# Performance work log

Hardware: AMD Instinct MI355X
Metric: run time of the kernel (lower is better)

Reference implementation:

```python
import jax, jax.numpy as jnp
import numpy as np

CHI, CHO, K, PAD = 64, 64, 3, 1
EPS = 1e-5


def setup_inputs() -> dict:
    key = jax.random.key(0)
    ks = jax.random.split(key, 4)
    B, H, W = 4, 128, 128
    x = jax.random.normal(ks[0], (B, CHI, H, W), jnp.float32)
    # conv_offset: produces 3*dg*K*K = 27 channels (o1, o2, mask); init small so offsets are modest
    w_off = jax.random.normal(ks[1], (3 * K * K, CHI, K, K), jnp.float32) * 0.01
    b_off = jnp.zeros((3 * K * K,), jnp.float32)
    # main deformable conv weight/bias
    w = jax.random.normal(ks[2], (CHO, CHI, K, K), jnp.float32) * (1.0 / np.sqrt(CHI * K * K))
    b = jnp.zeros((CHO,), jnp.float32)
    # BatchNorm affine params
    gamma = jnp.ones((CHO,), jnp.float32)
    beta = jnp.zeros((CHO,), jnp.float32)
    return {"x": x, "w_off": w_off, "b_off": b_off, "w": w, "b": b, "gamma": gamma, "beta": beta}


def _deform_conv(x, w_off, b_off, w, b):
    B, C, H, W_ = x.shape
    # offset/mask prediction: plain 3x3 conv, pad 1 -> [B, 27, H, W]
    off = jax.lax.conv_general_dilated(
        x, w_off, (1, 1), ((PAD, PAD), (PAD, PAD)),
        dimension_numbers=("NCHW", "OIHW", "NCHW")) + b_off[None, :, None, None]
    o1, o2, m = jnp.split(off, 3, axis=1)
    # mmcv DCNv2: offset = cat(o1, o2) -> [B, 2*K*K, H, W], interleaved (dy, dx) per tap
    offset = jnp.concatenate([o1, o2], axis=1).reshape(B, K * K, 2, H, W_)
    mask = jax.nn.sigmoid(m)                      # [B, 9, H, W]
    dy, dx = offset[:, :, 0], offset[:, :, 1]     # [B, 9, H, W]

    ky, kx = jnp.meshgrid(jnp.arange(K), jnp.arange(K), indexing="ij")
    ky = ky.reshape(1, K * K, 1, 1).astype(x.dtype)
    kx = kx.reshape(1, K * K, 1, 1).astype(x.dtype)
    hh = jnp.arange(H, dtype=x.dtype).reshape(1, 1, H, 1)
    ww = jnp.arange(W_, dtype=x.dtype).reshape(1, 1, 1, W_)
    py = hh - PAD + ky + dy                       # sampling row coords [B,9,H,W]
    px = ww - PAD + kx + dx                       # sampling col coords [B,9,H,W]

    y0 = jnp.floor(py)
    x0 = jnp.floor(px)
    wy = py - y0
    wx = px - x0

    x_flat = x.reshape(B, C, H * W_)

    def gather(yi, xi):
        # bilinear corner gather with zero padding outside the feature map
        valid = ((yi >= 0) & (yi < H) & (xi >= 0) & (xi < W_)).astype(x.dtype)
        yc = jnp.clip(yi, 0, H - 1).astype(jnp.int32)
        xc = jnp.clip(xi, 0, W_ - 1).astype(jnp.int32)
        idx = (yc * W_ + xc).reshape(B, 1, -1)
        v = jnp.take_along_axis(x_flat, idx, axis=2).reshape(B, C, K * K, H, W_)
        return v * valid[:, None]

    v00 = gather(y0, x0)
    v01 = gather(y0, x0 + 1)
    v10 = gather(y0 + 1, x0)
    v11 = gather(y0 + 1, x0 + 1)

    wy_ = wy[:, None]
    wx_ = wx[:, None]
    val = (v00 * (1 - wy_) * (1 - wx_) + v01 * (1 - wy_) * wx_
           + v10 * wy_ * (1 - wx_) + v11 * wy_ * wx_)
    val = val * mask[:, None]                     # modulated sampling [B,C,9,H,W]

    out = jnp.einsum("bckhw,ock->bohw", val, w.reshape(CHO, CHI, K * K))
    return out + b[None, :, None, None]


def reference(x, w_off, b_off, w, b, gamma, beta):
    y = _deform_conv(x, w_off, b_off, w, b)
    # BatchNorm2d (training-mode forward: batch statistics, biased variance)
    mean = y.mean(axis=(0, 2, 3))
    var = y.var(axis=(0, 2, 3))
    yhat = (y - mean[None, :, None, None]) * jax.lax.rsqrt(var[None, :, None, None] + EPS)
    return jax.nn.relu(yhat * gamma[None, :, None, None] + beta[None, :, None, None])
```

## Files before the change

### kernel.cpp

```cpp
#include <hip/hip_runtime.h>
#include <math.h>

#define CHI 64
#define CHO 64
#define HH 128
#define WW 128
#define NB 4
#define KK 9
#define NOFF 27
#define EPSV 1e-5f
#define PLANE (HH * WW)
#define SP 72

typedef float f32x4 __attribute__((ext_vector_type(4)));
typedef short bf16x8 __attribute__((ext_vector_type(8)));
typedef unsigned int u32x4 __attribute__((ext_vector_type(4)));

__device__ __forceinline__ unsigned short f2bf(float f) {
    unsigned u = __float_as_uint(f);
    u += 0x7fff + ((u >> 16) & 1);
    return (unsigned short)(u >> 16);
}
__device__ __forceinline__ float bfl(unsigned u) { return __uint_as_float(u << 16); }
__device__ __forceinline__ float bfh(unsigned u) { return __uint_as_float(u & 0xffff0000u); }

__global__ __launch_bounds__(256) void transpose_kernel(const float* __restrict__ x,
                                                        unsigned short* __restrict__ x_bf) {
    const int id = blockIdx.x;
    const int b  = id >> 7;
    const int y  = id & 127;
    const int t  = threadIdx.x;
    __shared__ unsigned short lt[128 * SP];

    const int ci = t >> 2, qx = t & 3;
    const float* src = x + ((size_t)(b * CHI + ci)) * PLANE + y * WW;
#pragma unroll
    for (int it = 0; it < 8; it++) {
        int xcol = (it * 4 + qx) * 4;
        float4 v = *(const float4*)(src + xcol);
        lt[(xcol + 0) * SP + ci] = f2bf(v.x);
        lt[(xcol + 1) * SP + ci] = f2bf(v.y);
        lt[(xcol + 2) * SP + ci] = f2bf(v.z);
        lt[(xcol + 3) * SP + ci] = f2bf(v.w);
    }
    __syncthreads();
    unsigned short* dst = x_bf + (size_t)id * (WW * 64);
#pragma unroll
    for (int it = 0; it < 4; it++) {
        int px  = it * 32 + (t >> 3);
        int ci8 = t & 7;
        u32x4 v = *(const u32x4*)&lt[px * SP + ci8 * 8];
        *(u32x4*)(dst + px * 64 + ci8 * 8) = v;
    }
}

__global__ __launch_bounds__(256) void prep_kernel(const float* __restrict__ w,
                                                   const float* __restrict__ w_off,
                                                   unsigned short* __restrict__ w_bf,
                                                   unsigned short* __restrict__ woA) {
    int i = blockIdx.x * 256 + threadIdx.x;
    {
        int j    = i & 7;
        int lane = (i >> 3) & 63;
        int ks   = (i >> 9) & 1;
        int ct   = (i >> 10) & 3;
        int kk   = i >> 12;
        int co   = ct * 16 + (lane & 15);
        int ci   = ks * 32 + ((lane >> 4) & 3) * 8 + j;
        w_bf[i]  = f2bf(w[(co * CHI + ci) * KK + kk]);
    }
    if (i < 18432) {
        int j    = i & 7;
        int lane = (i >> 3) & 63;
        int ct   = (i >> 9) & 1;
        int ks   = (i >> 10) & 1;
        int kk   = i >> 11;
        int c    = ct * 16 + (lane & 15);
        int ci   = ks * 32 + (lane >> 4) * 8 + j;
        woA[i]   = (c < NOFF) ? f2bf(w_off[(c * CHI + ci) * KK + kk]) : (unsigned short)0;
    }
}

__global__ __launch_bounds__(256) void off_conv_kernel(const unsigned short* __restrict__ x_bf,
                                                       const unsigned short* __restrict__ woA,
                                                       float* __restrict__ off) {
    const int id    = blockIdx.x;
    const int slot  = id & 7;
    const int b     = slot >> 1;
    const int rb    = id >> 3;
    const int h     = (slot & 1) * 64 + (rb >> 1);
    const int whalf = rb & 1;
    const int w0    = whalf * 64;
    const int tid   = threadIdx.x;
    const int lane  = tid & 63;
    const int wv    = __builtin_amdgcn_readfirstlane(tid >> 6);

    __shared__ __align__(16) unsigned short xs[3 * 66 * SP];

    const unsigned short* xb = x_bf + (size_t)b * (PLANE * 64);
#pragma unroll
    for (int ky = 0; ky < 3; ky++) {
        int hr = h - 1 + ky;
        for (int base = tid; base < 528; base += 256) {
            int col = base >> 3, ci8 = base & 7;
            int wc  = w0 - 1 + col;
            bool ok = ((unsigned)hr < HH) && ((unsigned)wc < WW);
            u32x4 v = {0u, 0u, 0u, 0u};
            if (ok) v = *(const u32x4*)(xb + ((size_t)(hr * WW + wc)) * 64 + ci8 * 8);
            *(u32x4*)&xs[(ky * 66 + col) * SP + ci8 * 8] = v;
        }
    }
    __syncthreads();

    const int quad = lane >> 4, pxin = lane & 15;
    f32x4 acc0 = {0.f, 0.f, 0.f, 0.f};
    f32x4 acc1 = {0.f, 0.f, 0.f, 0.f};

#pragma unroll 3
    for (int kk = 0; kk < KK; kk++) {
        const int ky = kk / 3, kx = kk - ky * 3;
#pragma unroll
        for (int ks = 0; ks < 2; ks++) {
            const bf16x8* wa = (const bf16x8*)woA + (size_t)((kk * 2 + ks) * 2) * 64;
            bf16x8 A0 = wa[lane];
            bf16x8 A1 = wa[64 + lane];
            bf16x8 B = *(const bf16x8*)&xs[(ky * 66 + wv * 16 + pxin + kx) * SP
                                           + ks * 32 + quad * 8];
            acc0 = __builtin_amdgcn_mfma_f32_16x16x32_bf16(A0, B, acc0, 0, 0, 0);
            acc1 = __builtin_amdgcn_mfma_f32_16x16x32_bf16(A1, B, acc1, 0, 0, 0);
        }
    }

    float* outp = off + ((size_t)b * NOFF * HH + h) * WW + w0 + wv * 16 + pxin;
#pragma unroll
    for (int r = 0; r < 4; r++) {
        int c0 = quad * 4 + r;
        outp[c0 * PLANE] = acc0[r];
        int c1 = 16 + quad * 4 + r;
        if (c1 < NOFF) outp[c1 * PLANE] = acc1[r];
    }
}

__global__ __launch_bounds__(256, 3) void deform_kernel(const unsigned short* __restrict__ x_bf,
                                                        const unsigned short* __restrict__ w_bf,
                                                        const float* __restrict__ off,
                                                        const float* __restrict__ b_off,
                                                        float* __restrict__ out,
                                                        float* __restrict__ pstats) {
    const int id    = blockIdx.x;
    const int slot  = id & 7;
    const int b     = slot >> 1;
    const int rb    = id >> 3;
    const int h     = (slot & 1) * 64 + (rb >> 1);
    const int whalf = rb & 1;
    const int tid   = threadIdx.x;
    const int lane  = tid & 63;
    const int wave  = __builtin_amdgcn_readfirstlane(tid >> 6);
    const int quad  = lane >> 4, pxin = lane & 15;

    f32x4 acc[4];
#pragma unroll
    for (int t = 0; t < 4; t++) acc[t] = (f32x4){0.f, 0.f, 0.f, 0.f};

    const int wpix = whalf * 64 + wave * 16 + pxin;
    const unsigned short* xbq = x_bf + (size_t)b * (PLANE * 64) + quad * 8;
    const float* offb = off + (size_t)b * NOFF * PLANE + h * WW + wpix;

    float dyv = offb[0 * PLANE]  + b_off[0];
    float dxv = offb[1 * PLANE]  + b_off[1];
    float mov = offb[18 * PLANE] + b_off[18];

#pragma unroll 3
    for (int kk = 0; kk < KK; kk++) {
        const int ky = kk / 3, kx = kk - ky * 3;
        float m   = 1.f / (1.f + __expf(-mov));
        float py  = (float)(h - 1 + ky) + dyv;
        float px_ = (float)(wpix - 1 + kx) + dxv;
        float fy0 = floorf(py), fx0 = floorf(px_);
        float wy = py - fy0, wx = px_ - fx0;
        int y0 = (int)fy0, x0 = (int)fx0;
        int y1 = y0 + 1, x1 = x0 + 1;
        bool vy0 = (unsigned)y0 < HH, vy1 = (unsigned)y1 < HH;
        bool vx0 = (unsigned)x0 < WW, vx1 = (unsigned)x1 < WW;
        float a00 = (vy0 && vx0) ? (1.f - wy) * (1.f - wx) * m : 0.f;
        float a01 = (vy0 && vx1) ? (1.f - wy) * wx * m : 0.f;
        float a10 = (vy1 && vx0) ? wy * (1.f - wx) * m : 0.f;
        float a11 = (vy1 && vx1) ? wy * wx * m : 0.f;
        int cy0 = min(max(y0, 0), HH - 1), cy1 = min(max(y1, 0), HH - 1);
        int cx0 = min(max(x0, 0), WW - 1), cx1 = min(max(x1, 0), WW - 1);
        const unsigned o00 = ((unsigned)(cy0 * WW + cx0)) << 6;
        const unsigned o01 = ((unsigned)(cy0 * WW + cx1)) << 6;
        const unsigned o10 = ((unsigned)(cy1 * WW + cx0)) << 6;
        const unsigned o11 = ((unsigned)(cy1 * WW + cx1)) << 6;

        u32x4 g00a = *(const u32x4*)(xbq + o00);
        u32x4 g01a = *(const u32x4*)(xbq + o01);
        u32x4 g10a = *(const u32x4*)(xbq + o10);
        u32x4 g11a = *(const u32x4*)(xbq + o11);
        u32x4 g00b = *(const u32x4*)(xbq + o00 + 32);
        u32x4 g01b = *(const u32x4*)(xbq + o01 + 32);
        u32x4 g10b = *(const u32x4*)(xbq + o10 + 32);
        u32x4 g11b = *(const u32x4*)(xbq + o11 + 32);

        if (kk + 1 < KK) {
            dyv = offb[(2 * kk + 2) * PLANE]  + b_off[2 * kk + 2];
            dxv = offb[(2 * kk + 3) * PLANE]  + b_off[2 * kk + 3];
            mov = offb[(18 + kk + 1) * PLANE] + b_off[18 + kk + 1];
        }

        const bf16x8* wb = (const bf16x8*)w_bf + (size_t)(kk * 8) * 64;
        bf16x8 A[8];
#pragma unroll
        for (int q = 0; q < 8; q++) A[q] = wb[q * 64 + lane];

        bf16x8 B0, B1;
#pragma unroll
        for (int d = 0; d < 4; d++) {
            float tl = a00 * bfl(g00a[d]) + a01 * bfl(g01a[d])
                     + a10 * bfl(g10a[d]) + a11 * bfl(g11a[d]);
            float th = a00 * bfh(g00a[d]) + a01 * bfh(g01a[d])
                     + a10 * bfh(g10a[d]) + a11 * bfh(g11a[d]);
            B0[2 * d]     = (short)f2bf(tl);
            B0[2 * d + 1] = (short)f2bf(th);
            float ul = a00 * bfl(g00b[d]) + a01 * bfl(g01b[d])
                     + a10 * bfl(g10b[d]) + a11 * bfl(g11b[d]);
            float uh = a00 * bfh(g00b[d]) + a01 * bfh(g01b[d])
                     + a10 * bfh(g10b[d]) + a11 * bfh(g11b[d]);
            B1[2 * d]     = (short)f2bf(ul);
            B1[2 * d + 1] = (short)f2bf(uh);
        }

#pragma unroll
        for (int t = 0; t < 4; t++) {
            acc[t] = __builtin_amdgcn_mfma_f32_16x16x32_bf16(A[t * 2 + 0], B0, acc[t], 0, 0, 0);
            acc[t] = __builtin_amdgcn_mfma_f32_16x16x32_bf16(A[t * 2 + 1], B1, acc[t], 0, 0, 0);
        }
    }

#pragma unroll
    for (int t = 0; t < 4; t++) {
#pragma unroll
        for (int r = 0; r < 4; r++) {
            int co = t * 16 + quad * 4 + r;
            out[(((size_t)b * CHO + co) * HH + h) * WW + whalf * 64 + wave * 16 + pxin] =
                acc[t][r];
        }
    }

    __shared__ float red[2][4][64];
#pragma unroll
    for (int t = 0; t < 4; t++) {
#pragma unroll
        for (int r = 0; r < 4; r++) {
            float s  = acc[t][r];
            float s2 = s * s;
#pragma unroll
            for (int mk = 1; mk < 16; mk <<= 1) {
                s  += __shfl_xor(s, mk, 64);
                s2 += __shfl_xor(s2, mk, 64);
            }
            if (pxin == 0) {
                int co = t * 16 + quad * 4 + r;
                red[0][wave][co] = s;
                red[1][wave][co] = s2;
            }
        }
    }
    __syncthreads();
    if (tid < 128) {
        int part = tid >> 6, idx = tid & 63;
        float v = red[part][0][idx] + red[part][1][idx]
                + red[part][2][idx] + red[part][3][idx];
        pstats[(size_t)(part * 64 + idx) * 1024 + id] = v;
    }
}

__global__ __launch_bounds__(256) void reduce_kernel(const float* __restrict__ pstats,
                                                     const float* __restrict__ bias,
                                                     float* __restrict__ stats) {
    const int co = blockIdx.x;
    const float* ps  = pstats + (size_t)co * 1024;
    const float* ps2 = pstats + (size_t)(64 + co) * 1024;
    float s = 0.f, s2 = 0.f;
    for (int i = threadIdx.x; i < 1024; i += 256) {
        s  += ps[i];
        s2 += ps2[i];
    }
#pragma unroll
    for (int o = 32; o > 0; o >>= 1) {
        s  += __shfl_down(s, o, 64);
        s2 += __shfl_down(s2, o, 64);
    }
    __shared__ float ls[8];
    int lane = threadIdx.x & 63, wv = threadIdx.x >> 6;
    if (lane == 0) { ls[wv] = s; ls[4 + wv] = s2; }
    __syncthreads();
    if (threadIdx.x == 0) {
        float S = ls[0] + ls[1] + ls[2] + ls[3];
        float S2 = ls[4] + ls[5] + ls[6] + ls[7];
        float bi = bias[co];
        stats[co]      = S + 65536.f * bi;
        stats[64 + co] = S2 + 2.f * bi * S + 65536.f * bi * bi;
    }
}

__global__ __launch_bounds__(256) void bn_kernel(float* __restrict__ y,
                                                 const float* __restrict__ bias,
                                                 const float* __restrict__ stats,
                                                 const float* __restrict__ gamma,
                                                 const float* __restrict__ beta) {
    size_t base = (size_t)blockIdx.x * 1024;
    int co = (int)((base >> 14) & 63);
    const float inv_n = 1.f / 65536.f;
    float mean = stats[co] * inv_n;
    float var  = stats[64 + co] * inv_n - mean * mean;
    float sc = gamma[co] * rsqrtf(var + EPSV);
    float sh = beta[co] - mean * sc;
    sh += bias[co] * sc;
    float4* p = (float4*)(y + base);
    float4 v = p[threadIdx.x];
    v.x = fmaxf(fmaf(v.x, sc, sh), 0.f);
    v.y = fmaxf(fmaf(v.y, sc, sh), 0.f);
    v.z = fmaxf(fmaf(v.z, sc, sh), 0.f);
    v.w = fmaxf(fmaf(v.w, sc, sh), 0.f);
    p[threadIdx.x] = v;
}

extern "C" void kernel_launch(void* const* d_in, const int* in_sizes, int n_in,
                              void* d_out, int out_size, void* d_ws, size_t ws_size,
                              hipStream_t stream) {
    const float* x     = (const float*)d_in[0];
    const float* w_off = (const float*)d_in[1];
    const float* b_off = (const float*)d_in[2];
    const float* wmat  = (const float*)d_in[3];
    const float* bvec  = (const float*)d_in[4];
    const float* gamma = (const float*)d_in[5];
    const float* beta  = (const float*)d_in[6];
    float* out = (float*)d_out;

    char* ws = (char*)d_ws;
    float* stats          = (float*)ws;
    unsigned short* w_bf  = (unsigned short*)(ws + 1024);
    unsigned short* woA   = (unsigned short*)(ws + 74752);
    float* off            = (float*)(ws + 139264);
    unsigned short* x_bf  = (unsigned short*)(ws + 7217152);
    float* pstats         = (float*)(ws + 15605760);

    transpose_kernel<<<512, 256, 0, stream>>>(x, x_bf);
    prep_kernel<<<144, 256, 0, stream>>>(wmat, w_off, w_bf, woA);
    off_conv_kernel<<<1024, 256, 0, stream>>>(x_bf, woA, off);
    deform_kernel<<<1024, 256, 0, stream>>>(x_bf, w_bf, off, b_off, out, pstats);
    reduce_kernel<<<64, 256, 0, stream>>>(pstats, bvec, stats);
    bn_kernel<<<4096, 256, 0, stream>>>(out, bvec, stats, gamma, beta);
}
```

Before: 146.4 us.

## Fuse offset conv into deform kernel and merge transpose with weight prep

The offset-prediction conv now runs inside the deformable conv kernel and keeps its 27 per-pixel outputs in shared memory, so the fp32 offset tensor is no longer written to and re-read from global memory. The shared-memory tile already holds the 3-row input halo and is reused for the offsets and the reduction scratch. Separately, the transpose and weight-prep kernels are merged into one launch, removing two kernel launches overall. In exchange, deform blocks do more work and take extra barriers, offset loads become shared-memory reads with a 28-float stride, and the old prefetch of the next tap's offsets is gone.

```diff
diff --git a/kernel.cpp b/kernel.cpp
--- a/kernel.cpp
+++ b/kernel.cpp
@@ -24,66 +24,69 @@
 __device__ __forceinline__ float bfl(unsigned u) { return __uint_as_float(u << 16); }
 __device__ __forceinline__ float bfh(unsigned u) { return __uint_as_float(u & 0xffff0000u); }
 
-__global__ __launch_bounds__(256) void transpose_kernel(const float* __restrict__ x,
-                                                        unsigned short* __restrict__ x_bf) {
-    const int id = blockIdx.x;
-    const int b  = id >> 7;
-    const int y  = id & 127;
-    const int t  = threadIdx.x;
-    __shared__ unsigned short lt[128 * SP];
-
-    const int ci = t >> 2, qx = t & 3;
-    const float* src = x + ((size_t)(b * CHI + ci)) * PLANE + y * WW;
-#pragma unroll
-    for (int it = 0; it < 8; it++) {
-        int xcol = (it * 4 + qx) * 4;
-        float4 v = *(const float4*)(src + xcol);
-        lt[(xcol + 0) * SP + ci] = f2bf(v.x);
-        lt[(xcol + 1) * SP + ci] = f2bf(v.y);
-        lt[(xcol + 2) * SP + ci] = f2bf(v.z);
-        lt[(xcol + 3) * SP + ci] = f2bf(v.w);
-    }
-    __syncthreads();
-    unsigned short* dst = x_bf + (size_t)id * (WW * 64);
-#pragma unroll
-    for (int it = 0; it < 4; it++) {
-        int px  = it * 32 + (t >> 3);
-        int ci8 = t & 7;
-        u32x4 v = *(const u32x4*)&lt[px * SP + ci8 * 8];
-        *(u32x4*)(dst + px * 64 + ci8 * 8) = v;
-    }
-}
-
-__global__ __launch_bounds__(256) void prep_kernel(const float* __restrict__ w,
+__global__ __launch_bounds__(256) void prep_kernel(const float* __restrict__ x,
+                                                   const float* __restrict__ w,
                                                    const float* __restrict__ w_off,
+                                                   unsigned short* __restrict__ x_bf,
                                                    unsigned short* __restrict__ w_bf,
                                                    unsigned short* __restrict__ woA) {
-    int i = blockIdx.x * 256 + threadIdx.x;
-    {
-        int j    = i & 7;
-        int lane = (i >> 3) & 63;
-        int ks   = (i >> 9) & 1;
-        int ct   = (i >> 10) & 3;
-        int kk   = i >> 12;
-        int co   = ct * 16 + (lane & 15);
-        int ci   = ks * 32 + ((lane >> 4) & 3) * 8 + j;
-        w_bf[i]  = f2bf(w[(co * CHI + ci) * KK + kk]);
-    }
-    if (i < 18432) {
-        int j    = i & 7;
-        int lane = (i >> 3) & 63;
-        int ct   = (i >> 9) & 1;
-        int ks   = (i >> 10) & 1;
-        int kk   = i >> 11;
-        int c    = ct * 16 + (lane & 15);
-        int ci   = ks * 32 + (lane >> 4) * 8 + j;
-        woA[i]   = (c < NOFF) ? f2bf(w_off[(c * CHI + ci) * KK + kk]) : (unsigned short)0;
-    }
-}
-
-__global__ __launch_bounds__(256) void off_conv_kernel(const unsigned short* __restrict__ x_bf,
-                                                       const unsigned short* __restrict__ woA,
-                                                       float* __restrict__ off) {
+    __shared__ unsigned short lt[128 * SP];
+    if (blockIdx.x < 512) {
+        const int id = blockIdx.x;
+        const int b  = id >> 7;
+        const int y  = id & 127;
+        const int t  = threadIdx.x;
+        const int ci = t >> 2, qx = t & 3;
+        const float* src = x + ((size_t)(b * CHI + ci)) * PLANE + y * WW;
+#pragma unroll
+        for (int it = 0; it < 8; it++) {
+            int xcol = (it * 4 + qx) * 4;
+            float4 v = *(const float4*)(src + xcol);
+            lt[(xcol + 0) * SP + ci] = f2bf(v.x);
+            lt[(xcol + 1) * SP + ci] = f2bf(v.y);
+            lt[(xcol + 2) * SP + ci] = f2bf(v.z);
+            lt[(xcol + 3) * SP + ci] = f2bf(v.w);
+        }
+        __syncthreads();
+        unsigned short* dst = x_bf + (size_t)id * (WW * 64);
+#pragma unroll
+        for (int it = 0; it < 4; it++) {
+            int px  = it * 32 + (t >> 3);
+            int ci8 = t & 7;
+            u32x4 v = *(const u32x4*)&lt[px * SP + ci8 * 8];
+            *(u32x4*)(dst + px * 64 + ci8 * 8) = v;
+        }
+    } else {
+        int i = (blockIdx.x - 512) * 256 + threadIdx.x;
+        {
+            int j    = i & 7;
+            int lane = (i >> 3) & 63;
+            int ks   = (i >> 9) & 1;
+            int ct   = (i >> 10) & 3;
+            int kk   = i >> 12;
+            int co   = ct * 16 + (lane & 15);
+            int ci   = ks * 32 + ((lane >> 4) & 3) * 8 + j;
+            w_bf[i]  = f2bf(w[(co * CHI + ci) * KK + kk]);
+        }
+        if (i < 18432) {
+            int j    = i & 7;
+            int lane = (i >> 3) & 63;
+            int ct   = (i >> 9) & 1;
+            int ks   = (i >> 10) & 1;
+            int kk   = i >> 11;
+            int c    = ct * 16 + (lane & 15);
+            int ci   = ks * 32 + (lane >> 4) * 8 + j;
+            woA[i]   = (c < NOFF) ? f2bf(w_off[(c * CHI + ci) * KK + kk]) : (unsigned short)0;
+        }
+    }
+}
+
+__global__ __launch_bounds__(256, 3) void deform_kernel(const unsigned short* __restrict__ x_bf,
+                                                        const unsigned short* __restrict__ w_bf,
+                                                        const unsigned short* __restrict__ woA,
+                                                        const float* __restrict__ b_off,
+                                                        float* __restrict__ out,
+                                                        float* __restrict__ pstats) {
     const int id    = blockIdx.x;
     const int slot  = id & 7;
     const int b     = slot >> 1;
@@ -93,9 +96,13 @@
     const int w0    = whalf * 64;
     const int tid   = threadIdx.x;
     const int lane  = tid & 63;
-    const int wv    = __builtin_amdgcn_readfirstlane(tid >> 6);
+    const int wave  = __builtin_amdgcn_readfirstlane(tid >> 6);
+    const int quad  = lane >> 4, pxin = lane & 15;
+    const int pxl   = wave * 16 + pxin;
 
     __shared__ __align__(16) unsigned short xs[3 * 66 * SP];
+    float* offs = (float*)xs;
+    float* red  = (float*)(xs + 4096);
 
     const unsigned short* xb = x_bf + (size_t)b * (PLANE * 64);
 #pragma unroll
@@ -112,10 +119,8 @@
     }
     __syncthreads();
 
-    const int quad = lane >> 4, pxin = lane & 15;
-    f32x4 acc0 = {0.f, 0.f, 0.f, 0.f};
-    f32x4 acc1 = {0.f, 0.f, 0.f, 0.f};
-
+    f32x4 oacc0 = {0.f, 0.f, 0.f, 0.f};
+    f32x4 oacc1 = {0.f, 0.f, 0.f, 0.f};
 #pragma unroll 3
     for (int kk = 0; kk < KK; kk++) {
         const int ky = kk / 3, kx = kk - ky * 3;
@@ -124,55 +129,37 @@
             const bf16x8* wa = (const bf16x8*)woA + (size_t)((kk * 2 + ks) * 2) * 64;
             bf16x8 A0 = wa[lane];
             bf16x8 A1 = wa[64 + lane];
-            bf16x8 B = *(const bf16x8*)&xs[(ky * 66 + wv * 16 + pxin + kx) * SP
+            bf16x8 B = *(const bf16x8*)&xs[(ky * 66 + wave * 16 + pxin + kx) * SP
                                            + ks * 32 + quad * 8];
-            acc0 = __builtin_amdgcn_mfma_f32_16x16x32_bf16(A0, B, acc0, 0, 0, 0);
-            acc1 = __builtin_amdgcn_mfma_f32_16x16x32_bf16(A1, B, acc1, 0, 0, 0);
-        }
-    }
-
-    float* outp = off + ((size_t)b * NOFF * HH + h) * WW + w0 + wv * 16 + pxin;
+            oacc0 = __builtin_amdgcn_mfma_f32_16x16x32_bf16(A0, B, oacc0, 0, 0, 0);
+            oacc1 = __builtin_amdgcn_mfma_f32_16x16x32_bf16(A1, B, oacc1, 0, 0, 0);
+        }
+    }
+    __syncthreads();
+
 #pragma unroll
     for (int r = 0; r < 4; r++) {
         int c0 = quad * 4 + r;
-        outp[c0 * PLANE] = acc0[r];
+        offs[pxl * 28 + c0] = oacc0[r];
         int c1 = 16 + quad * 4 + r;
-        if (c1 < NOFF) outp[c1 * PLANE] = acc1[r];
-    }
-}
-
-__global__ __launch_bounds__(256, 3) void deform_kernel(const unsigned short* __restrict__ x_bf,
-                                                        const unsigned short* __restrict__ w_bf,
-                                                        const float* __restrict__ off,
-                                                        const float* __restrict__ b_off,
-                                                        float* __restrict__ out,
-                                                        float* __restrict__ pstats) {
-    const int id    = blockIdx.x;
-    const int slot  = id & 7;
-    const int b     = slot >> 1;
-    const int rb    = id >> 3;
-    const int h     = (slot & 1) * 64 + (rb >> 1);
-    const int whalf = rb & 1;
-    const int tid   = threadIdx.x;
-    const int lane  = tid & 63;
-    const int wave  = __builtin_amdgcn_readfirstlane(tid >> 6);
-    const int quad  = lane >> 4, pxin = lane & 15;
+        if (c1 < NOFF) offs[pxl * 28 + c1] = oacc1[r];
+    }
+    __syncthreads();
 
     f32x4 acc[4];
 #pragma unroll
     for (int t = 0; t < 4; t++) acc[t] = (f32x4){0.f, 0.f, 0.f, 0.f};
 
-    const int wpix = whalf * 64 + wave * 16 + pxin;
-    const unsigned short* xbq = x_bf + (size_t)b * (PLANE * 64) + quad * 8;
-    const float* offb = off + (size_t)b * NOFF * PLANE + h * WW + wpix;
-
-    float dyv = offb[0 * PLANE]  + b_off[0];
-    float dxv = offb[1 * PLANE]  + b_off[1];
-    float mov = offb[18 * PLANE] + b_off[18];
+    const int wpix = w0 + wave * 16 + pxin;
+    const unsigned short* xbq = xb + quad * 8;
 
 #pragma unroll 3
     for (int kk = 0; kk < KK; kk++) {
         const int ky = kk / 3, kx = kk - ky * 3;
+        float dyv = offs[pxl * 28 + 2 * kk]     + b_off[2 * kk];
+        float dxv = offs[pxl * 28 + 2 * kk + 1] + b_off[2 * kk + 1];
+        float mov = offs[pxl * 28 + 18 + kk]    + b_off[18 + kk];
+
         float m   = 1.f / (1.f + __expf(-mov));
         float py  = (float)(h - 1 + ky) + dyv;
         float px_ = (float)(wpix - 1 + kx) + dxv;
@@ -202,12 +189,6 @@
         u32x4 g10b = *(const u32x4*)(xbq + o10 + 32);
         u32x4 g11b = *(const u32x4*)(xbq + o11 + 32);
 
-        if (kk + 1 < KK) {
-            dyv = offb[(2 * kk + 2) * PLANE]  + b_off[2 * kk + 2];
-            dxv = offb[(2 * kk + 3) * PLANE]  + b_off[2 * kk + 3];
-            mov = offb[(18 + kk + 1) * PLANE] + b_off[18 + kk + 1];
-        }
-
         const bf16x8* wb = (const bf16x8*)w_bf + (size_t)(kk * 8) * 64;
         bf16x8 A[8];
 #pragma unroll
@@ -242,12 +223,11 @@
 #pragma unroll
         for (int r = 0; r < 4; r++) {
             int co = t * 16 + quad * 4 + r;
-            out[(((size_t)b * CHO + co) * HH + h) * WW + whalf * 64 + wave * 16 + pxin] =
+            out[(((size_t)b * CHO + co) * HH + h) * WW + w0 + wave * 16 + pxin] =
                 acc[t][r];
         }
     }
 
-    __shared__ float red[2][4][64];
 #pragma unroll
     for (int t = 0; t < 4; t++) {
 #pragma unroll
@@ -261,16 +241,16 @@
             }
             if (pxin == 0) {
                 int co = t * 16 + quad * 4 + r;
-                red[0][wave][co] = s;
-                red[1][wave][co] = s2;
+                red[(0 * 4 + wave) * 64 + co] = s;
+                red[(1 * 4 + wave) * 64 + co] = s2;
             }
         }
     }
     __syncthreads();
     if (tid < 128) {
         int part = tid >> 6, idx = tid & 63;
-        float v = red[part][0][idx] + red[part][1][idx]
-                + red[part][2][idx] + red[part][3][idx];
+        float v = red[(part * 4 + 0) * 64 + idx] + red[(part * 4 + 1) * 64 + idx]
+                + red[(part * 4 + 2) * 64 + idx] + red[(part * 4 + 3) * 64 + idx];
         pstats[(size_t)(part * 64 + idx) * 1024 + id] = v;
     }
 }
@@ -342,14 +322,11 @@
     float* stats          = (float*)ws;
     unsigned short* w_bf  = (unsigned short*)(ws + 1024);
     unsigned short* woA   = (unsigned short*)(ws + 74752);
-    float* off            = (float*)(ws + 139264);
-    unsigned short* x_bf  = (unsigned short*)(ws + 7217152);
-    float* pstats         = (float*)(ws + 15605760);
-
-    transpose_kernel<<<512, 256, 0, stream>>>(x, x_bf);
-    prep_kernel<<<144, 256, 0, stream>>>(wmat, w_off, w_bf, woA);
-    off_conv_kernel<<<1024, 256, 0, stream>>>(x_bf, woA, off);
-    deform_kernel<<<1024, 256, 0, stream>>>(x_bf, w_bf, off, b_off, out, pstats);
+    unsigned short* x_bf  = (unsigned short*)(ws + 139264);
+    float* pstats         = (float*)(ws + 8527872);
+
+    prep_kernel<<<656, 256, 0, stream>>>(x, wmat, w_off, x_bf, w_bf, woA);
+    deform_kernel<<<1024, 256, 0, stream>>>(x_bf, w_bf, woA, b_off, out, pstats);
     reduce_kernel<<<64, 256, 0, stream>>>(pstats, bvec, stats);
     bn_kernel<<<4096, 256, 0, stream>>>(out, bvec, stats, gamma, beta);
 }
```

New measurement: 154.2 us. +5.3%, slower.
